# Kernel tuning notes

Measured on AMD Instinct MI355X. Metric: run time of the kernel, lower is better.

Reference implementation:

```python
import jax, jax.numpy as jnp
from jax import lax
import numpy as np

# CenterNet decode config
B, C, H, W = 16, 80, 128, 128  # batch, classes, feature-map H/W (512 input / down_ratio 4)
K = 100                        # top-K detections per image
DOWN = 4.0                     # down_ratio: feature-map coords -> input-image coords


def setup_inputs() -> dict:
    key = jax.random.key(0)
    k1, k2, k3 = jax.random.split(key, 3)
    return {
        "output_heatmap": jax.random.normal(k1, (B, C, H, W), dtype=jnp.float32),
        "output_bbox": jax.random.uniform(k2, (B, 2, H, W), dtype=jnp.float32) * 32.0,  # wh head
        "output_offset": jax.random.uniform(k3, (B, 2, H, W), dtype=jnp.float32),       # sub-pixel offset head
        "image_id": jnp.arange(B, dtype=jnp.int32),
    }


def reference(output_heatmap, output_bbox, output_offset, image_id):
    # 1) peak scores
    hm = jax.nn.sigmoid(output_heatmap)  # [B,C,H,W]
    # 2) 3x3 maxpool NMS: keep only local maxima
    hmax = lax.reduce_window(hm, -jnp.inf, lax.max,
                             window_dimensions=(1, 1, 3, 3),
                             window_strides=(1, 1, 1, 1),
                             padding='SAME')
    hm = jnp.where(hmax == hm, hm, jnp.zeros((), hm.dtype))
    # 3) per-image top-K over all classes and positions
    scores, inds = lax.top_k(hm.reshape(B, C * H * W), K)  # [B,K]
    cls = (inds // (H * W)).astype(jnp.float32)             # [B,K]
    sp = inds % (H * W)                                     # spatial index in [0, H*W)
    ys = (sp // W).astype(jnp.float32)
    xs = (sp % W).astype(jnp.float32)
    # 4) sparse gather of offset and wh at the K peak locations
    off = jnp.take_along_axis(output_offset.reshape(B, 2, H * W), sp[:, None, :], axis=2)  # [B,2,K]
    wh = jnp.take_along_axis(output_bbox.reshape(B, 2, H * W), sp[:, None, :], axis=2)     # [B,2,K]
    cx = xs + off[:, 0]
    cy = ys + off[:, 1]
    w = wh[:, 0]
    h = wh[:, 1]
    # 5) decode to corner boxes in input-image coordinates
    boxes = jnp.stack([cx - w / 2, cy - h / 2, cx + w / 2, cy + h / 2], axis=-1) * DOWN  # [B,K,4]
    img = jnp.broadcast_to(image_id[:, None].astype(jnp.float32), (B, K))
    # detections: [image_id, x1, y1, x2, y2, score, class] -> [B,K,7]
    det = jnp.concatenate([img[..., None], boxes, scores[..., None], cls[..., None]], axis=-1)
    return det
```

## Files before the change

kernel.cpp:

```cpp
#include <hip/hip_runtime.h>

#define BB 16
#define CC 80
#define HWs 16384
#define KK 100
#define NBIN 2048
#define NBLK (BB * CC * 2)
#define NSLOT 160
#define BCAP 1152
#define SBCAP 64

#define OFF_BHIST 0
#define OFF_PBCNT 131072
#define OFF_PSCNT 141312
#define OFF_SURV  151552
#define OFF_REC   806912

__device__ __forceinline__ unsigned okey(float f) {
    unsigned u = __float_as_uint(f);
    return (u & 0x80000000u) ? ~u : (u | 0x80000000u);
}

__global__ __launch_bounds__(256) void zero_hist_kernel(int4* __restrict__ bhist) {
    int i = blockIdx.x * 256 + threadIdx.x;
    if (i < BB * NBIN / 4) bhist[i] = make_int4(0, 0, 0, 0);
}

__global__ __launch_bounds__(256) void nms_kernel(const float* __restrict__ hm,
                                                  unsigned* __restrict__ rec,
                                                  int* __restrict__ pbcnt,
                                                  int* __restrict__ bhist) {
    __shared__ int hist[NBIN];
    __shared__ unsigned sbuf[BCAP];
    __shared__ int s_n;
    const int blk = blockIdx.x;
    const int plane = blk >> 1;
    const int half = blk & 1;
    const int b = plane / CC;
    const int c = plane - b * CC;
    const int t = threadIdx.x;
    const int sx = t & 31;
    const int x0 = sx << 2;
    const int y0 = (half << 6) + ((t >> 5) << 3);
    const float4* __restrict__ src4 =
        reinterpret_cast<const float4*>(hm + (size_t)plane * HWs);

    for (int i = t; i < NBIN; i += 256) hist[i] = 0;
    if (t == 0) s_n = 0;
    __syncthreads();

    float4 w[10];
#pragma unroll
    for (int i = 0; i < 10; ++i) {
        int rr = y0 - 1 + i;
        rr = rr < 0 ? 0 : (rr > 127 ? 127 : rr);
        w[i] = src4[(rr << 5) + sx];
    }
    __builtin_amdgcn_sched_barrier(0);

    auto hmax3 = [&](const float4& a) -> float4 {
        float vm1 = __shfl_up(a.w, 1, 32);
        float vp4 = __shfl_down(a.x, 1, 32);
        if (sx == 0) vm1 = a.x;
        if (sx == 31) vp4 = a.w;
        float4 h;
        h.x = fmaxf(fmaxf(vm1, a.x), a.y);
        h.y = fmaxf(fmaxf(a.x, a.y), a.z);
        h.z = fmaxf(fmaxf(a.y, a.z), a.w);
        h.w = fmaxf(fmaxf(a.z, a.w), vp4);
        return h;
    };

    float4 hm1 = hmax3(w[0]);
    float4 h0  = hmax3(w[1]);
#pragma unroll
    for (int r = 0; r < 8; ++r) {
        float4 hp1 = hmax3(w[r + 2]);
        float vv[4] = { w[r + 1].x, w[r + 1].y, w[r + 1].z, w[r + 1].w };
        float mm[4] = { fmaxf(fmaxf(hm1.x, h0.x), hp1.x),
                        fmaxf(fmaxf(hm1.y, h0.y), hp1.y),
                        fmaxf(fmaxf(hm1.z, h0.z), hp1.z),
                        fmaxf(fmaxf(hm1.w, h0.w), hp1.w) };
#pragma unroll
        for (int j = 0; j < 4; ++j) {
            if (vv[j] >= mm[j]) {
                int sl = atomicAdd(&s_n, 1);
                unsigned bin = okey(vv[j]) >> 21;
                unsigned idx = ((unsigned)c << 14)
                             | ((unsigned)(y0 + r) << 7) | (unsigned)(x0 + j);
                if (sl < BCAP) sbuf[sl] = (bin << 21) | idx;
            }
        }
        hm1 = h0; h0 = hp1;
    }
    __syncthreads();
    int n = s_n; if (n > BCAP) n = BCAP;

    for (int i = t; i < n; i += 256) atomicAdd(&hist[sbuf[i] >> 21], 1);
    __syncthreads();
    for (int i = t; i < NBIN; i += 256) {
        int hv = hist[i];
        if (hv) atomicAdd(&bhist[b * NBIN + i], hv);
    }
    unsigned* __restrict__ rb = rec + (size_t)blk * BCAP;
    for (int i = t; i < n; i += 256) rb[i] = sbuf[i];
    if (t == 0) pbcnt[blk] = n;
}

__global__ __launch_bounds__(256) void filter_kernel(const unsigned* __restrict__ rec,
                                                     const int* __restrict__ pbcnt,
                                                     const int* __restrict__ bhist,
                                                     unsigned* __restrict__ surv,
                                                     int* __restrict__ pscnt) {
    __shared__ int csum[256];
    __shared__ int s_cut, s_n;
    const int blk = blockIdx.x;
    const int b = blk / NSLOT;
    const int t = threadIdx.x;

    int h[8]; int chunk = 0;
#pragma unroll
    for (int j = 0; j < 8; ++j) {
        h[j] = bhist[b * NBIN + (t << 3) + j];
        chunk += h[j];
    }
    csum[t] = chunk;
    if (t == 0) { s_cut = 0; s_n = 0; }
    __syncthreads();
    for (int off = 1; off < 256; off <<= 1) {
        int v = (t + off < 256) ? csum[t + off] : 0;
        __syncthreads();
        csum[t] += v;
        __syncthreads();
    }
    if (csum[0] > KK) {
        int running = (t < 255) ? csum[t + 1] : 0;
        if (csum[t] >= KK && running < KK) {
            for (int j = 7; j >= 0; --j) {
                running += h[j];
                if (running >= KK) { s_cut = (t << 3) + j; break; }
            }
        }
    }
    __syncthreads();
    const unsigned cutb = (unsigned)s_cut;

    int n = pbcnt[blk]; if (n > BCAP) n = BCAP;
    const unsigned* __restrict__ rb = rec + (size_t)blk * BCAP;
    unsigned* __restrict__ sb = surv + (size_t)blk * SBCAP;
    for (int i = t; i < n; i += 256) {
        unsigned rv = rb[i];
        if ((rv >> 21) >= cutb) {
            int sl = atomicAdd(&s_n, 1);
            if (sl < SBCAP) sb[sl] = rv & 0x1FFFFFu;
        }
    }
    __syncthreads();
    if (t == 0) pscnt[blk] = s_n > SBCAP ? SBCAP : s_n;
}

__global__ __launch_bounds__(256) void topk_kernel(const unsigned* __restrict__ surv,
                                                   const int* __restrict__ pscnt,
                                                   const float* __restrict__ hm,
                                                   const float* __restrict__ bbox,
                                                   const float* __restrict__ offs,
                                                   const int* __restrict__ image_id,
                                                   float* __restrict__ out) {
    __shared__ int lcnt[NSLOT];
    __shared__ unsigned uidx[2048];
    __shared__ unsigned long long list[2048];
    __shared__ int s_n;
    const int b = blockIdx.x;
    const int t = threadIdx.x;
    const float* __restrict__ hb = hm + (size_t)b * CC * HWs;

    if (t < NSLOT) lcnt[t] = pscnt[b * NSLOT + t];
    if (t == 0) s_n = 0;
    __syncthreads();

    for (int s = t; s < NSLOT; s += 256) {
        int cs = lcnt[s]; if (cs > SBCAP) cs = SBCAP;
        if (cs) {
            int base = atomicAdd(&s_n, cs);
            const unsigned* __restrict__ sb = surv + ((size_t)b * NSLOT + s) * SBCAP;
            for (int k = 0; k < cs; ++k)
                if (base + k < 2048) uidx[base + k] = sb[k];
        }
    }
    __syncthreads();
    int n = s_n; if (n > 2048) n = 2048;

    for (int i = t; i < n; i += 256) {
        unsigned idx = uidx[i];
        float lv = hb[idx];
        float s = 1.0f / (1.0f + expf(-lv));
        list[i] = ((unsigned long long)__float_as_uint(s) << 32) | (unsigned)(~idx);
    }
    int P = 128;
    while (P < n) P <<= 1;
    for (int i = n + t; i < P; i += 256) list[i] = 0ull;
    __syncthreads();

    for (int ksz = 2; ksz <= P; ksz <<= 1) {
        for (int j = ksz >> 1; j > 0; j >>= 1) {
            for (int i = t; i < P; i += 256) {
                int ixj = i ^ j;
                if (ixj > i) {
                    unsigned long long a = list[i], bb2 = list[ixj];
                    bool desc = ((i & ksz) == 0);
                    if (desc ? (a < bb2) : (a > bb2)) { list[i] = bb2; list[ixj] = a; }
                }
            }
            __syncthreads();
        }
    }

    if (t < KK) {
        float s = 0.0f; unsigned idx = 0;
        if (t < n) {
            unsigned long long cv = list[t];
            s = __uint_as_float((unsigned)(cv >> 32));
            idx = ~(unsigned)(cv & 0xFFFFFFFFu) & 0x1FFFFFu;
        }
        unsigned sp = idx & (HWs - 1);
        float cls = (float)(idx >> 14);
        float ysf = (float)(sp >> 7);
        float xsf = (float)(sp & 127);
        const float* __restrict__ ob  = offs + (size_t)b * 2 * HWs;
        const float* __restrict__ bbx = bbox + (size_t)b * 2 * HWs;
        float cx = xsf + ob[sp];
        float cy = ysf + ob[HWs + sp];
        float w = bbx[sp];
        float h = bbx[HWs + sp];
        float* row = out + ((size_t)b * KK + t) * 7;
        row[0] = (float)image_id[b];
        row[1] = (cx - w * 0.5f) * 4.0f;
        row[2] = (cy - h * 0.5f) * 4.0f;
        row[3] = (cx + w * 0.5f) * 4.0f;
        row[4] = (cy + h * 0.5f) * 4.0f;
        row[5] = s;
        row[6] = cls;
    }
}

extern "C" void kernel_launch(void* const* d_in, const int* in_sizes, int n_in,
                              void* d_out, int out_size, void* d_ws, size_t ws_size,
                              hipStream_t stream) {
    const float* hm      = (const float*)d_in[0];
    const float* bbox    = (const float*)d_in[1];
    const float* offset  = (const float*)d_in[2];
    const int*   img_id  = (const int*)d_in[3];
    float* out = (float*)d_out;

    char* ws = (char*)d_ws;
    int*      bhist = (int*)(ws + OFF_BHIST);
    int*      pbcnt = (int*)(ws + OFF_PBCNT);
    int*      pscnt = (int*)(ws + OFF_PSCNT);
    unsigned* surv  = (unsigned*)(ws + OFF_SURV);
    unsigned* rec   = (unsigned*)(ws + OFF_REC);

    zero_hist_kernel<<<32, 256, 0, stream>>>((int4*)bhist);
    nms_kernel<<<NBLK, 256, 0, stream>>>(hm, rec, pbcnt, bhist);
    filter_kernel<<<NBLK, 256, 0, stream>>>(rec, pbcnt, bhist, surv, pscnt);
    topk_kernel<<<BB, 256, 0, stream>>>(surv, pscnt, hm, bbox, offset, img_id, out);
}
```

Before: 60.34 us.

## Hoist per-image cutoff scan into own kernel and split NMS rows into two strips

```diff
diff --git a/kernel.cpp b/kernel.cpp
--- a/kernel.cpp
+++ b/kernel.cpp
@@ -11,10 +11,11 @@
 #define SBCAP 64
 
 #define OFF_BHIST 0
-#define OFF_PBCNT 131072
-#define OFF_PSCNT 141312
-#define OFF_SURV  151552
-#define OFF_REC   806912
+#define OFF_CUT   131072
+#define OFF_PBCNT 131136
+#define OFF_PSCNT 141376
+#define OFF_SURV  151616
+#define OFF_REC   806976
 
 __device__ __forceinline__ unsigned okey(float f) {
     unsigned u = __float_as_uint(f);
@@ -41,7 +42,9 @@
     const int t = threadIdx.x;
     const int sx = t & 31;
     const int x0 = sx << 2;
-    const int y0 = (half << 6) + ((t >> 5) << 3);
+    const int g = t >> 5;
+    const int yA = (half << 6) + (g << 2);
+    const int yB = yA + 32;
     const float4* __restrict__ src4 =
         reinterpret_cast<const float4*>(hm + (size_t)plane * HWs);
 
@@ -49,12 +52,13 @@
     if (t == 0) s_n = 0;
     __syncthreads();
 
-    float4 w[10];
-#pragma unroll
-    for (int i = 0; i < 10; ++i) {
-        int rr = y0 - 1 + i;
-        rr = rr < 0 ? 0 : (rr > 127 ? 127 : rr);
-        w[i] = src4[(rr << 5) + sx];
+    float4 wa[6], wb[6];
+#pragma unroll
+    for (int i = 0; i < 6; ++i) {
+        int ra = yA - 1 + i; ra = ra < 0 ? 0 : (ra > 127 ? 127 : ra);
+        int rb = yB - 1 + i; rb = rb < 0 ? 0 : (rb > 127 ? 127 : rb);
+        wa[i] = src4[(ra << 5) + sx];
+        wb[i] = src4[(rb << 5) + sx];
     }
     __builtin_amdgcn_sched_barrier(0);
 
@@ -71,28 +75,33 @@
         return h;
     };
 
-    float4 hm1 = hmax3(w[0]);
-    float4 h0  = hmax3(w[1]);
-#pragma unroll
-    for (int r = 0; r < 8; ++r) {
-        float4 hp1 = hmax3(w[r + 2]);
-        float vv[4] = { w[r + 1].x, w[r + 1].y, w[r + 1].z, w[r + 1].w };
-        float mm[4] = { fmaxf(fmaxf(hm1.x, h0.x), hp1.x),
-                        fmaxf(fmaxf(hm1.y, h0.y), hp1.y),
-                        fmaxf(fmaxf(hm1.z, h0.z), hp1.z),
-                        fmaxf(fmaxf(hm1.w, h0.w), hp1.w) };
-#pragma unroll
-        for (int j = 0; j < 4; ++j) {
-            if (vv[j] >= mm[j]) {
-                int sl = atomicAdd(&s_n, 1);
-                unsigned bin = okey(vv[j]) >> 21;
-                unsigned idx = ((unsigned)c << 14)
-                             | ((unsigned)(y0 + r) << 7) | (unsigned)(x0 + j);
-                if (sl < BCAP) sbuf[sl] = (bin << 21) | idx;
+    auto process = [&](const float4* w, int y0) {
+        float4 hm1 = hmax3(w[0]);
+        float4 h0  = hmax3(w[1]);
+#pragma unroll
+        for (int r = 0; r < 4; ++r) {
+            float4 hp1 = hmax3(w[r + 2]);
+            float vv[4] = { w[r + 1].x, w[r + 1].y, w[r + 1].z, w[r + 1].w };
+            float mm[4] = { fmaxf(fmaxf(hm1.x, h0.x), hp1.x),
+                            fmaxf(fmaxf(hm1.y, h0.y), hp1.y),
+                            fmaxf(fmaxf(hm1.z, h0.z), hp1.z),
+                            fmaxf(fmaxf(hm1.w, h0.w), hp1.w) };
+#pragma unroll
+            for (int j = 0; j < 4; ++j) {
+                if (vv[j] >= mm[j]) {
+                    int sl = atomicAdd(&s_n, 1);
+                    unsigned bin = okey(vv[j]) >> 21;
+                    unsigned idx = ((unsigned)c << 14)
+                                 | ((unsigned)(y0 + r) << 7) | (unsigned)(x0 + j);
+                    if (sl < BCAP) sbuf[sl] = (bin << 21) | idx;
+                }
             }
-        }
-        hm1 = h0; h0 = hp1;
-    }
+            hm1 = h0; h0 = hp1;
+        }
+    };
+    process(wa, yA);
+    process(wb, yB);
+
     __syncthreads();
     int n = s_n; if (n > BCAP) n = BCAP;
 
@@ -107,15 +116,11 @@
     if (t == 0) pbcnt[blk] = n;
 }
 
-__global__ __launch_bounds__(256) void filter_kernel(const unsigned* __restrict__ rec,
-                                                     const int* __restrict__ pbcnt,
-                                                     const int* __restrict__ bhist,
-                                                     unsigned* __restrict__ surv,
-                                                     int* __restrict__ pscnt) {
+__global__ __launch_bounds__(256) void cut_kernel(const int* __restrict__ bhist,
+                                                  int* __restrict__ cut) {
     __shared__ int csum[256];
-    __shared__ int s_cut, s_n;
-    const int blk = blockIdx.x;
-    const int b = blk / NSLOT;
+    __shared__ int s_cut;
+    const int b = blockIdx.x;
     const int t = threadIdx.x;
 
     int h[8]; int chunk = 0;
@@ -125,7 +130,7 @@
         chunk += h[j];
     }
     csum[t] = chunk;
-    if (t == 0) { s_cut = 0; s_n = 0; }
+    if (t == 0) s_cut = 0;
     __syncthreads();
     for (int off = 1; off < 256; off <<= 1) {
         int v = (t + off < 256) ? csum[t + off] : 0;
@@ -143,9 +148,23 @@
         }
     }
     __syncthreads();
-    const unsigned cutb = (unsigned)s_cut;
+    if (t == 0) cut[b] = s_cut;
+}
+
+__global__ __launch_bounds__(256) void filter_kernel(const unsigned* __restrict__ rec,
+                                                     const int* __restrict__ pbcnt,
+                                                     const int* __restrict__ cut,
+                                                     unsigned* __restrict__ surv,
+                                                     int* __restrict__ pscnt) {
+    __shared__ int s_n;
+    const int blk = blockIdx.x;
+    const int b = blk / NSLOT;
+    const int t = threadIdx.x;
+    if (t == 0) s_n = 0;
+    __syncthreads();
 
     int n = pbcnt[blk]; if (n > BCAP) n = BCAP;
+    const unsigned cutb = (unsigned)cut[b];
     const unsigned* __restrict__ rb = rec + (size_t)blk * BCAP;
     unsigned* __restrict__ sb = surv + (size_t)blk * SBCAP;
     for (int i = t; i < n; i += 256) {
@@ -254,6 +273,7 @@
 
     char* ws = (char*)d_ws;
     int*      bhist = (int*)(ws + OFF_BHIST);
+    int*      cut   = (int*)(ws + OFF_CUT);
     int*      pbcnt = (int*)(ws + OFF_PBCNT);
     int*      pscnt = (int*)(ws + OFF_PSCNT);
     unsigned* surv  = (unsigned*)(ws + OFF_SURV);
@@ -261,6 +281,7 @@
 
     zero_hist_kernel<<<32, 256, 0, stream>>>((int4*)bhist);
     nms_kernel<<<NBLK, 256, 0, stream>>>(hm, rec, pbcnt, bhist);
-    filter_kernel<<<NBLK, 256, 0, stream>>>(rec, pbcnt, bhist, surv, pscnt);
+    cut_kernel<<<BB, 256, 0, stream>>>(bhist, cut);
+    filter_kernel<<<NBLK, 256, 0, stream>>>(rec, pbcnt, cut, surv, pscnt);
     topk_kernel<<<BB, 256, 0, stream>>>(surv, pscnt, hm, bbox, offset, img_id, out);
 }
```

Result: no change. 61.15 us (+1.3%).

## Replace shared-memory atomics in NMS with wave-scan compaction and separate histogram kernel

Applied to the files above, without the earlier changes.

```diff
diff --git a/kernel.cpp b/kernel.cpp
--- a/kernel.cpp
+++ b/kernel.cpp
@@ -7,14 +7,14 @@
 #define NBIN 2048
 #define NBLK (BB * CC * 2)
 #define NSLOT 160
-#define BCAP 1152
+#define WCAP 288
 #define SBCAP 64
 
 #define OFF_BHIST 0
-#define OFF_PBCNT 131072
-#define OFF_PSCNT 141312
-#define OFF_SURV  151552
-#define OFF_REC   806912
+#define OFF_PWCNT 131072
+#define OFF_PSCNT 172032
+#define OFF_SURV  182272
+#define OFF_REC   837632
 
 __device__ __forceinline__ unsigned okey(float f) {
     unsigned u = __float_as_uint(f);
@@ -28,33 +28,30 @@
 
 __global__ __launch_bounds__(256) void nms_kernel(const float* __restrict__ hm,
                                                   unsigned* __restrict__ rec,
-                                                  int* __restrict__ pbcnt,
-                                                  int* __restrict__ bhist) {
-    __shared__ int hist[NBIN];
-    __shared__ unsigned sbuf[BCAP];
-    __shared__ int s_n;
+                                                  int* __restrict__ pwcnt) {
     const int blk = blockIdx.x;
     const int plane = blk >> 1;
     const int half = blk & 1;
     const int b = plane / CC;
     const int c = plane - b * CC;
     const int t = threadIdx.x;
+    const int lane = t & 63;
+    const int wid = t >> 6;
     const int sx = t & 31;
     const int x0 = sx << 2;
-    const int y0 = (half << 6) + ((t >> 5) << 3);
+    const int g = t >> 5;
+    const int yA = (half << 6) + (g << 2);
+    const int yB = yA + 32;
     const float4* __restrict__ src4 =
         reinterpret_cast<const float4*>(hm + (size_t)plane * HWs);
 
-    for (int i = t; i < NBIN; i += 256) hist[i] = 0;
-    if (t == 0) s_n = 0;
-    __syncthreads();
-
-    float4 w[10];
-#pragma unroll
-    for (int i = 0; i < 10; ++i) {
-        int rr = y0 - 1 + i;
-        rr = rr < 0 ? 0 : (rr > 127 ? 127 : rr);
-        w[i] = src4[(rr << 5) + sx];
+    float4 wa[6], wb[6];
+#pragma unroll
+    for (int i = 0; i < 6; ++i) {
+        int ra = yA - 1 + i; ra = ra < 0 ? 0 : (ra > 127 ? 127 : ra);
+        int rb = yB - 1 + i; rb = rb < 0 ? 0 : (rb > 127 ? 127 : rb);
+        wa[i] = src4[(ra << 5) + sx];
+        wb[i] = src4[(rb << 5) + sx];
     }
     __builtin_amdgcn_sched_barrier(0);
 
@@ -71,44 +68,99 @@
         return h;
     };
 
-    float4 hm1 = hmax3(w[0]);
-    float4 h0  = hmax3(w[1]);
-#pragma unroll
-    for (int r = 0; r < 8; ++r) {
-        float4 hp1 = hmax3(w[r + 2]);
-        float vv[4] = { w[r + 1].x, w[r + 1].y, w[r + 1].z, w[r + 1].w };
-        float mm[4] = { fmaxf(fmaxf(hm1.x, h0.x), hp1.x),
-                        fmaxf(fmaxf(hm1.y, h0.y), hp1.y),
-                        fmaxf(fmaxf(hm1.z, h0.z), hp1.z),
-                        fmaxf(fmaxf(hm1.w, h0.w), hp1.w) };
-#pragma unroll
-        for (int j = 0; j < 4; ++j) {
-            if (vv[j] >= mm[j]) {
-                int sl = atomicAdd(&s_n, 1);
-                unsigned bin = okey(vv[j]) >> 21;
-                unsigned idx = ((unsigned)c << 14)
-                             | ((unsigned)(y0 + r) << 7) | (unsigned)(x0 + j);
-                if (sl < BCAP) sbuf[sl] = (bin << 21) | idx;
+    auto mask_of = [&](const float4* w) -> unsigned {
+        unsigned pm = 0;
+        float4 hm1 = hmax3(w[0]);
+        float4 h0  = hmax3(w[1]);
+#pragma unroll
+        for (int r = 0; r < 4; ++r) {
+            float4 hp1 = hmax3(w[r + 2]);
+            if (w[r + 1].x >= fmaxf(fmaxf(hm1.x, h0.x), hp1.x)) pm |= 1u << (r * 4 + 0);
+            if (w[r + 1].y >= fmaxf(fmaxf(hm1.y, h0.y), hp1.y)) pm |= 1u << (r * 4 + 1);
+            if (w[r + 1].z >= fmaxf(fmaxf(hm1.z, h0.z), hp1.z)) pm |= 1u << (r * 4 + 2);
+            if (w[r + 1].w >= fmaxf(fmaxf(hm1.w, h0.w), hp1.w)) pm |= 1u << (r * 4 + 3);
+            hm1 = h0; h0 = hp1;
+        }
+        return pm;
+    };
+
+    const unsigned pmA = mask_of(wa);
+    const unsigned pmB = mask_of(wb);
+
+    int cntA = __popc(pmA), cntB = __popc(pmB);
+    int scA = cntA, scB = cntB;
+#pragma unroll
+    for (int off = 1; off < 64; off <<= 1) {
+        int nA = __shfl_up(scA, off, 64);
+        int nB = __shfl_up(scB, off, 64);
+        if (lane >= off) { scA += nA; scB += nB; }
+    }
+    const int totalA = __shfl(scA, 63, 64);
+    const int totalB = __shfl(scB, 63, 64);
+    const int baseA = scA - cntA;
+    const int baseB = totalA + scB - cntB;
+
+    unsigned* __restrict__ wr = rec + (size_t)((blk << 2) + wid) * WCAP;
+
+    auto emit = [&](const float4* w, unsigned pm, int base, int y0) {
+#pragma unroll
+        for (int r = 0; r < 4; ++r) {
+#pragma unroll
+            for (int j = 0; j < 4; ++j) {
+                unsigned bit = 1u << (r * 4 + j);
+                if (pm & bit) {
+                    float lv = (j == 0) ? w[r + 1].x : (j == 1) ? w[r + 1].y
+                             : (j == 2) ? w[r + 1].z : w[r + 1].w;
+                    int slot = base + __popc(pm & (bit - 1));
+                    unsigned idx = ((unsigned)c << 14)
+                                 | ((unsigned)(y0 + r) << 7) | (unsigned)(x0 + j);
+                    if (slot < WCAP)
+                        wr[slot] = ((okey(lv) >> 21) << 21) | idx;
+                }
             }
         }
-        hm1 = h0; h0 = hp1;
-    }
-    __syncthreads();
-    int n = s_n; if (n > BCAP) n = BCAP;
-
-    for (int i = t; i < n; i += 256) atomicAdd(&hist[sbuf[i] >> 21], 1);
+    };
+    emit(wa, pmA, baseA, yA);
+    emit(wb, pmB, baseB, yB);
+
+    if (lane == 63) {
+        int tot = totalA + totalB;
+        pwcnt[(blk << 2) + wid] = tot > WCAP ? WCAP : tot;
+    }
+}
+
+__global__ __launch_bounds__(256) void hist_kernel(const unsigned* __restrict__ rec,
+                                                   const int* __restrict__ pwcnt,
+                                                   int* __restrict__ bhist) {
+    __shared__ int hist[NBIN];
+    __shared__ int lcnt[64];
+    const int bx = blockIdx.x;
+    const int b = bx / 10;
+    const int p = bx - b * 10;
+    const int slot0 = b * 640 + p * 64;
+    const int t = threadIdx.x;
+
+    for (int i = t; i < NBIN; i += 256) hist[i] = 0;
+    if (t < 64) {
+        int n = pwcnt[slot0 + t];
+        lcnt[t] = n > WCAP ? WCAP : n;
+    }
+    __syncthreads();
+
+    for (int s = 0; s < 64; ++s) {
+        int n = lcnt[s];
+        const unsigned* __restrict__ rb = rec + (size_t)(slot0 + s) * WCAP;
+        for (int i = t; i < n; i += 256) atomicAdd(&hist[rb[i] >> 21], 1);
+    }
     __syncthreads();
     for (int i = t; i < NBIN; i += 256) {
         int hv = hist[i];
         if (hv) atomicAdd(&bhist[b * NBIN + i], hv);
     }
-    unsigned* __restrict__ rb = rec + (size_t)blk * BCAP;
-    for (int i = t; i < n; i += 256) rb[i] = sbuf[i];
-    if (t == 0) pbcnt[blk] = n;
 }
 
 __global__ __launch_bounds__(256) void filter_kernel(const unsigned* __restrict__ rec,
-                                                     const int* __restrict__ pbcnt,
+                                                     const int* __restrict__ pwcnt,
                                                      const int* __restrict__ bhist,
                                                      unsigned* __restrict__ surv,
                                                      int* __restrict__ pscnt) {
@@ -145,14 +197,18 @@
     __syncthreads();
     const unsigned cutb = (unsigned)s_cut;
 
-    int n = pbcnt[blk]; if (n > BCAP) n = BCAP;
-    const unsigned* __restrict__ rb = rec + (size_t)blk * BCAP;
     unsigned* __restrict__ sb = surv + (size_t)blk * SBCAP;
-    for (int i = t; i < n; i += 256) {
-        unsigned rv = rb[i];
-        if ((rv >> 21) >= cutb) {
-            int sl = atomicAdd(&s_n, 1);
-            if (sl < SBCAP) sb[sl] = rv & 0x1FFFFFu;
+#pragma unroll
+    for (int k = 0; k < 4; ++k) {
+        int ws = (blk << 2) + k;
+        int n = pwcnt[ws]; if (n > WCAP) n = WCAP;
+        const unsigned* __restrict__ rb = rec + (size_t)ws * WCAP;
+        for (int i = t; i < n; i += 256) {
+            unsigned rv = rb[i];
+            if ((rv >> 21) >= cutb) {
+                int sl = atomicAdd(&s_n, 1);
+                if (sl < SBCAP) sb[sl] = rv & 0x1FFFFFu;
+            }
         }
     }
     __syncthreads();
@@ -254,13 +310,14 @@
 
     char* ws = (char*)d_ws;
     int*      bhist = (int*)(ws + OFF_BHIST);
-    int*      pbcnt = (int*)(ws + OFF_PBCNT);
+    int*      pwcnt = (int*)(ws + OFF_PWCNT);
     int*      pscnt = (int*)(ws + OFF_PSCNT);
     unsigned* surv  = (unsigned*)(ws + OFF_SURV);
     unsigned* rec   = (unsigned*)(ws + OFF_REC);
 
     zero_hist_kernel<<<32, 256, 0, stream>>>((int4*)bhist);
-    nms_kernel<<<NBLK, 256, 0, stream>>>(hm, rec, pbcnt, bhist);
-    filter_kernel<<<NBLK, 256, 0, stream>>>(rec, pbcnt, bhist, surv, pscnt);
+    nms_kernel<<<NBLK, 256, 0, stream>>>(hm, rec, pwcnt);
+    hist_kernel<<<BB * 10, 256, 0, stream>>>(rec, pwcnt, bhist);
+    filter_kernel<<<NBLK, 256, 0, stream>>>(rec, pwcnt, bhist, surv, pscnt);
     topk_kernel<<<BB, 256, 0, stream>>>(surv, pscnt, hm, bbox, offset, img_id, out);
 }
```

Result: slower. 82.21 us (+36.2%).
